# Performance work log

Measured on AMD Instinct MI355X. Metric: run time of the kernel, lower is better.

## Reference

```python
import jax, jax.numpy as jnp
import numpy as np

N, E, D, L = 50000, 800000, 128, 4


def setup_inputs() -> dict:
    key = jax.random.key(0)
    k0, k1, k2, k3 = jax.random.split(key, 4)
    x = jax.random.normal(k0, (N, D), dtype=jnp.float32)
    edge_index = jax.random.randint(k1, (2, E), 0, N, dtype=jnp.int32)
    # per-layer GCNConv weights [L, D, D] and biases [L, D]
    W = jax.random.normal(k2, (L, D, D), dtype=jnp.float32) * (1.0 / np.sqrt(D))
    b = jax.random.normal(k3, (L, D), dtype=jnp.float32) * 0.01
    batch_index = jnp.zeros((N,), dtype=jnp.int32)
    node_rankings = jnp.zeros((N,), dtype=jnp.int32)
    return {"x": x, "edge_index": edge_index, "batch_index": batch_index,
            "node_rankings": node_rankings, "W": W, "b": b}


def reference(x, edge_index, batch_index, node_rankings, W, b):
    # NullControl contributes 0; dropout_rate=0 / eval -> identity.
    n = x.shape[0]
    loops = jnp.arange(n, dtype=edge_index.dtype)
    row = jnp.concatenate([edge_index[0], loops])  # sources (with self-loops)
    col = jnp.concatenate([edge_index[1], loops])  # destinations
    # symmetric GCN normalization: deg over destinations, norm = d_i^-1/2 d_j^-1/2
    deg = jax.ops.segment_sum(jnp.ones_like(row, dtype=x.dtype), col, num_segments=n)
    dinv = jnp.where(deg > 0, jax.lax.rsqrt(deg), 0.0)
    norm = dinv[row] * dinv[col]  # [E+N]
    for l in range(W.shape[0]):
        h = x @ W[l]                      # [N, D] dense transform
        msg = h[row] * norm[:, None]      # [E+N, D] gathered, scaled messages
        agg = jax.ops.segment_sum(msg, col, num_segments=n)  # scatter-add
        x = jax.nn.relu(agg + b[l])       # control(=0) + bias + relu
    return x
```

## Files before the change

kernel.cpp:

```cpp
#include <hip/hip_runtime.h>

#define D 128
#define NLAYERS 4

typedef unsigned short ushort_t;
typedef unsigned int uint_t;
typedef __attribute__((ext_vector_type(8))) short short8;
typedef __attribute__((ext_vector_type(4))) float f32x4;

__device__ __forceinline__ ushort_t f2bf(float f) {
    uint_t u = __float_as_uint(f);
    u += 0x7FFFu + ((u >> 16) & 1u);
    return (ushort_t)(u >> 16);
}
__device__ __forceinline__ float bf_lo(uint_t u) {
    return __uint_as_float(u << 16);
}
__device__ __forceinline__ float bf_hi(uint_t u) {
    return __uint_as_float(u & 0xFFFF0000u);
}
__device__ __forceinline__ uint_t pack2(float a, float b) {
    return (uint_t)f2bf(a) | ((uint_t)f2bf(b) << 16);
}


__global__ void k_count_deg(const int* __restrict__ dsts, int E,
                            int* __restrict__ deg, int* __restrict__ slot) {
    int i = blockIdx.x * blockDim.x + threadIdx.x;
    if (i < E) slot[i] = atomicAdd(&deg[dsts[i]], 1);
}

__global__ void k_scan1(const int* __restrict__ deg, int n, int* __restrict__ out,
                        int* __restrict__ partials, float* __restrict__ dinv) {
    __shared__ int wsum[4];
    int tid = threadIdx.x;
    int base = blockIdx.x * 1024 + tid * 4;
    int d0 = (base + 0 < n) ? deg[base + 0] : 0;
    int d1 = (base + 1 < n) ? deg[base + 1] : 0;
    int d2 = (base + 2 < n) ? deg[base + 2] : 0;
    int d3 = (base + 3 < n) ? deg[base + 3] : 0;
    if (base + 0 < n) dinv[base + 0] = rsqrtf((float)(d0 + 1));
    if (base + 1 < n) dinv[base + 1] = rsqrtf((float)(d1 + 1));
    if (base + 2 < n) dinv[base + 2] = rsqrtf((float)(d2 + 1));
    if (base + 3 < n) dinv[base + 3] = rsqrtf((float)(d3 + 1));
    int s = d0 + d1 + d2 + d3;
    int lane = tid & 63;
    int incl = s;
    #pragma unroll
    for (int off = 1; off < 64; off <<= 1) {
        int y = __shfl_up(incl, off);
        if (lane >= off) incl += y;
    }
    int wid = tid >> 6;
    if (lane == 63) wsum[wid] = incl;
    __syncthreads();
    int wprev = 0;
    for (int w = 0; w < wid; w++) wprev += wsum[w];
    int excl = wprev + (incl - s);
    if (base + 0 < n) out[base + 0] = excl;
    if (base + 1 < n) out[base + 1] = excl + d0;
    if (base + 2 < n) out[base + 2] = excl + d0 + d1;
    if (base + 3 < n) out[base + 3] = excl + d0 + d1 + d2;
    if (tid == 255) partials[blockIdx.x] = wprev + incl;
}

__global__ void k_scan2(int* partials, int nb) {
    if (threadIdx.x == 0 && blockIdx.x == 0) {
        int acc = 0;
        for (int i = 0; i < nb; i++) { int t = partials[i]; partials[i] = acc; acc += t; }
    }
}

__global__ void k_scan3(int* __restrict__ row_ptr, const int* __restrict__ partials,
                        int n, int E) {
    int i = blockIdx.x * blockDim.x + threadIdx.x;
    if (i < n) row_ptr[i] += partials[i >> 10];
    if (i == 0) row_ptr[n] = E;
}

__global__ void k_place(const int* __restrict__ srcs, const int* __restrict__ dsts, int E,
                        const int* __restrict__ row_ptr, const int* __restrict__ slot,
                        const float* __restrict__ dinv, int2* __restrict__ ew) {
    int i = blockIdx.x * blockDim.x + threadIdx.x;
    if (i >= E) return;
    int c = dsts[i], r = srcs[i];
    int pos = row_ptr[c] + slot[i];
    int2 v;
    v.x = r;
    v.y = __float_as_int(dinv[r]);
    ew[pos] = v;
}

__global__ void k_wprep(const float* __restrict__ W, ushort_t* __restrict__ Wt_hi,
                        ushort_t* __restrict__ Wt_lo) {
    int t = blockIdx.x * 256 + threadIdx.x;
    int l = t >> 14;
    int k = (t >> 7) & 127;
    int nn = t & 127;
    float w = W[((size_t)l << 14) + k * 128 + nn];
    ushort_t hi = f2bf(w);
    float wf = __uint_as_float((uint_t)hi << 16);
    ushort_t lo = f2bf(w - wf);
    size_t o = ((size_t)l << 14) + nn * 128 + k;
    Wt_hi[o] = hi;
    Wt_lo[o] = lo;
}

__global__ void k_tobf16(const float* __restrict__ x, ushort_t* __restrict__ xh,
                         int total4) {
    int i = blockIdx.x * blockDim.x + threadIdx.x;
    if (i >= total4) return;
    float4 v = ((const float4*)x)[i];
    uint2 o;
    o.x = pack2(v.x, v.y);
    o.y = pack2(v.z, v.w);
    ((uint2*)xh)[i] = o;
}

__global__ __launch_bounds__(256) void k_aggregate(
    const ushort_t* __restrict__ xh, const int* __restrict__ row_ptr,
    const int2* __restrict__ ew, const float* __restrict__ dinv,
    ushort_t* __restrict__ s, int n) {
    int gwave = (blockIdx.x * 256 + threadIdx.x) >> 6;
    if (gwave >= n) return;
    int lane = threadIdx.x & 63;
    int sub = lane >> 4;
    int t = lane & 15;
    int node = gwave;
    float di = dinv[node];

    float acc[8];
    {
        uint4 v = *(const uint4*)(xh + (size_t)node * D + t * 8);
        float w = (sub == 0) ? di : 0.f;
        acc[0] = w * bf_lo(v.x); acc[1] = w * bf_hi(v.x);
        acc[2] = w * bf_lo(v.y); acc[3] = w * bf_hi(v.y);
        acc[4] = w * bf_lo(v.z); acc[5] = w * bf_hi(v.z);
        acc[6] = w * bf_lo(v.w); acc[7] = w * bf_hi(v.w);
    }
    int e = row_ptr[node], end = row_ptr[node + 1];
    for (; e + 16 <= end; e += 16) {
        int2 g0 = ew[e + sub];
        int2 g1 = ew[e + 4 + sub];
        int2 g2 = ew[e + 8 + sub];
        int2 g3 = ew[e + 12 + sub];
        uint4 v0 = *(const uint4*)(xh + (size_t)g0.x * D + t * 8);
        uint4 v1 = *(const uint4*)(xh + (size_t)g1.x * D + t * 8);
        uint4 v2 = *(const uint4*)(xh + (size_t)g2.x * D + t * 8);
        uint4 v3 = *(const uint4*)(xh + (size_t)g3.x * D + t * 8);
        float w0 = __int_as_float(g0.y);
        float w1 = __int_as_float(g1.y);
        float w2 = __int_as_float(g2.y);
        float w3 = __int_as_float(g3.y);
        acc[0] += w0 * bf_lo(v0.x); acc[1] += w0 * bf_hi(v0.x);
        acc[2] += w0 * bf_lo(v0.y); acc[3] += w0 * bf_hi(v0.y);
        acc[4] += w0 * bf_lo(v0.z); acc[5] += w0 * bf_hi(v0.z);
        acc[6] += w0 * bf_lo(v0.w); acc[7] += w0 * bf_hi(v0.w);
        acc[0] += w1 * bf_lo(v1.x); acc[1] += w1 * bf_hi(v1.x);
        acc[2] += w1 * bf_lo(v1.y); acc[3] += w1 * bf_hi(v1.y);
        acc[4] += w1 * bf_lo(v1.z); acc[5] += w1 * bf_hi(v1.z);
        acc[6] += w1 * bf_lo(v1.w); acc[7] += w1 * bf_hi(v1.w);
        acc[0] += w2 * bf_lo(v2.x); acc[1] += w2 * bf_hi(v2.x);
        acc[2] += w2 * bf_lo(v2.y); acc[3] += w2 * bf_hi(v2.y);
        acc[4] += w2 * bf_lo(v2.z); acc[5] += w2 * bf_hi(v2.z);
        acc[6] += w2 * bf_lo(v2.w); acc[7] += w2 * bf_hi(v2.w);
        acc[0] += w3 * bf_lo(v3.x); acc[1] += w3 * bf_hi(v3.x);
        acc[2] += w3 * bf_lo(v3.y); acc[3] += w3 * bf_hi(v3.y);
        acc[4] += w3 * bf_lo(v3.z); acc[5] += w3 * bf_hi(v3.z);
        acc[6] += w3 * bf_lo(v3.w); acc[7] += w3 * bf_hi(v3.w);
    }
    for (; e < end; e += 4) {
        int rem = end - e;
        int k = (sub < rem) ? sub : 0;
        int2 g = ew[e + k];
        float w = (sub < rem) ? __int_as_float(g.y) : 0.f;
        uint4 v = *(const uint4*)(xh + (size_t)g.x * D + t * 8);
        acc[0] += w * bf_lo(v.x); acc[1] += w * bf_hi(v.x);
        acc[2] += w * bf_lo(v.y); acc[3] += w * bf_hi(v.y);
        acc[4] += w * bf_lo(v.z); acc[5] += w * bf_hi(v.z);
        acc[6] += w * bf_lo(v.w); acc[7] += w * bf_hi(v.w);
    }
    #pragma unroll
    for (int q = 0; q < 8; q++) {
        acc[q] += __shfl_xor(acc[q], 16);
        acc[q] += __shfl_xor(acc[q], 32);
    }
    if (sub == 0) {
        ushort_t* dst = s + (size_t)node * D + t * 8;
        uint4 o;
        o.x = pack2(di * acc[0], di * acc[1]);
        o.y = pack2(di * acc[2], di * acc[3]);
        o.z = pack2(di * acc[4], di * acc[5]);
        o.w = pack2(di * acc[6], di * acc[7]);
        *(uint4*)dst = o;
    }
}

__global__ __launch_bounds__(256) void k_gemm_mfma(
    const ushort_t* __restrict__ A, const ushort_t* __restrict__ Wt_hi,
    const ushort_t* __restrict__ Wt_lo, const float* __restrict__ bias,
    float* __restrict__ out_f32, ushort_t* __restrict__ out_bf, int n) {
    int tid = threadIdx.x;
    int wave = tid >> 6;
    int lane = tid & 63;
    int lg = lane >> 4;
    int lr = lane & 15;
    int base_row = blockIdx.x * 128 + wave * 32;

    short8 a[2][4];
    #pragma unroll
    for (int st = 0; st < 2; st++) {
        int r = base_row + st * 16 + lr;
        if (r > n - 1) r = n - 1;
        const ushort_t* ap = A + (size_t)r * D + lg * 8;
        #pragma unroll
        for (int k0 = 0; k0 < 4; k0++)
            a[st][k0] = *(const short8*)(ap + k0 * 32);
    }

    f32x4 acc[2][8];
    #pragma unroll
    for (int st = 0; st < 2; st++)
        #pragma unroll
        for (int nt = 0; nt < 8; nt++)
            acc[st][nt] = (f32x4){0.f, 0.f, 0.f, 0.f};

    #pragma unroll
    for (int nt = 0; nt < 8; nt++) {
        const ushort_t* wh = Wt_hi + (size_t)(nt * 16 + lr) * D + lg * 8;
        const ushort_t* wl = Wt_lo + (size_t)(nt * 16 + lr) * D + lg * 8;
        #pragma unroll
        for (int k0 = 0; k0 < 4; k0++) {
            short8 bh = *(const short8*)(wh + k0 * 32);
            short8 bl = *(const short8*)(wl + k0 * 32);
            acc[0][nt] = __builtin_amdgcn_mfma_f32_16x16x32_bf16(a[0][k0], bh, acc[0][nt], 0, 0, 0);
            acc[0][nt] = __builtin_amdgcn_mfma_f32_16x16x32_bf16(a[0][k0], bl, acc[0][nt], 0, 0, 0);
            acc[1][nt] = __builtin_amdgcn_mfma_f32_16x16x32_bf16(a[1][k0], bh, acc[1][nt], 0, 0, 0);
            acc[1][nt] = __builtin_amdgcn_mfma_f32_16x16x32_bf16(a[1][k0], bl, acc[1][nt], 0, 0, 0);
        }
    }

    #pragma unroll
    for (int nt = 0; nt < 8; nt++) {
        int col = nt * 16 + lr;
        float bv = bias[col];
        #pragma unroll
        for (int st = 0; st < 2; st++) {
            #pragma unroll
            for (int r = 0; r < 4; r++) {
                int grow = base_row + st * 16 + lg * 4 + r;
                if (grow < n) {
                    float o = fmaxf(acc[st][nt][r] + bv, 0.f);
                    if (out_bf) out_bf[(size_t)grow * D + col] = f2bf(o);
                    else out_f32[(size_t)grow * D + col] = o;
                }
            }
        }
    }
}


extern "C" void kernel_launch(void* const* d_in, const int* in_sizes, int n_in,
                              void* d_out, int out_size, void* d_ws, size_t ws_size,
                              hipStream_t stream) {
    const float* x   = (const float*)d_in[0];
    const int* eidx  = (const int*)d_in[1];
    const float* W   = (const float*)d_in[4];
    const float* b   = (const float*)d_in[5];
    float* out       = (float*)d_out;

    const int N = in_sizes[0] / D;
    const int E = in_sizes[1] / 2;
    const int* srcs = eidx;
    const int* dsts = eidx + E;

    char* ws = (char*)d_ws;
    size_t off = 0;
    auto alloc = [&](size_t bytes) -> void* {
        void* p = ws + off;
        off = (off + bytes + 511) & ~(size_t)511;
        return p;
    };
    int*      deg      = (int*)alloc((size_t)N * 4);
    float*    dinv     = (float*)alloc((size_t)N * 4);
    int*      row_ptr  = (int*)alloc((size_t)(N + 1) * 4);
    int*      partials = (int*)alloc(256 * 4);
    int2*     ew       = (int2*)alloc((size_t)E * 8);
    ushort_t* s_buf    = (ushort_t*)alloc((size_t)N * D * 2);
    ushort_t* xh0      = (ushort_t*)alloc((size_t)N * D * 2);
    ushort_t* xh1      = (ushort_t*)alloc((size_t)N * D * 2);
    ushort_t* wt_hi    = (ushort_t*)alloc((size_t)NLAYERS * D * D * 2);
    ushort_t* wt_lo    = (ushort_t*)alloc((size_t)NLAYERS * D * D * 2);
    int*      slot     = (int*)s_buf;
    (void)ws_size; (void)n_in; (void)out_size;

    hipMemsetAsync(deg, 0, (size_t)N * 4, stream);

    int tE = (E + 255) / 256;
    int tN = (N + 255) / 256;
    int nbScan = (N + 1023) / 1024;

    k_count_deg<<<tE, 256, 0, stream>>>(dsts, E, deg, slot);
    k_scan1<<<nbScan, 256, 0, stream>>>(deg, N, row_ptr, partials, dinv);
    k_scan2<<<1, 64, 0, stream>>>(partials, nbScan);
    k_scan3<<<tN, 256, 0, stream>>>(row_ptr, partials, N, E);
    k_place<<<tE, 256, 0, stream>>>(srcs, dsts, E, row_ptr, slot, dinv, ew);
    k_wprep<<<(NLAYERS * D * D) / 256, 256, 0, stream>>>(W, wt_hi, wt_lo);

    int total4 = N * D / 4;
    k_tobf16<<<(total4 + 255) / 256, 256, 0, stream>>>(x, xh0, total4);

    int aggBlocks = (N + 3) / 4;
    int gemmBlocks = (N + 127) / 128;

    const ushort_t* xin = xh0;
    for (int l = 0; l < NLAYERS; l++) {
        k_aggregate<<<aggBlocks, 256, 0, stream>>>(xin, row_ptr, ew, dinv, s_buf, N);
        bool last = (l == NLAYERS - 1);
        ushort_t* xout = last ? nullptr : ((l & 1) ? xh0 : xh1);
        k_gemm_mfma<<<gemmBlocks, 256, 0, stream>>>(
            s_buf, wt_hi + (size_t)l * D * D, wt_lo + (size_t)l * D * D,
            b + (size_t)l * D, last ? out : nullptr, xout, N);
        xin = xout;
    }
}
```

Before: 387.2 us.

## Pre-scale features by dinv, pad CSR rows to multiples of four, fuse prep kernels

Features are stored pre-multiplied by the source node's dinv, and the GEMM epilogue applies dinv to its output. Edge weights therefore drop out and the CSR holds only 4-byte indices. Each row, including its self-loop, is padded to a multiple of four with a dummy zero row, so the aggregation can load four indices at once with an int4 and skip the per-edge multiply and tail masking. The scan, placement, weight prep and bf16 conversion kernels are merged into fewer launches. The cost is extra padded gathers of the zero row and slightly different bf16 rounding, since scaling now happens before quantisation.

```diff
diff --git a/kernel.cpp b/kernel.cpp
--- a/kernel.cpp
+++ b/kernel.cpp
@@ -30,20 +30,24 @@
     if (i < E) slot[i] = atomicAdd(&deg[dsts[i]], 1);
 }
 
-__global__ void k_scan1(const int* __restrict__ deg, int n, int* __restrict__ out,
+__global__ void k_scan1(const int* __restrict__ deg, int n, int* __restrict__ prow,
                         int* __restrict__ partials, float* __restrict__ dinv) {
     __shared__ int wsum[4];
     int tid = threadIdx.x;
     int base = blockIdx.x * 1024 + tid * 4;
-    int d0 = (base + 0 < n) ? deg[base + 0] : 0;
-    int d1 = (base + 1 < n) ? deg[base + 1] : 0;
-    int d2 = (base + 2 < n) ? deg[base + 2] : 0;
-    int d3 = (base + 3 < n) ? deg[base + 3] : 0;
-    if (base + 0 < n) dinv[base + 0] = rsqrtf((float)(d0 + 1));
-    if (base + 1 < n) dinv[base + 1] = rsqrtf((float)(d1 + 1));
-    if (base + 2 < n) dinv[base + 2] = rsqrtf((float)(d2 + 1));
-    if (base + 3 < n) dinv[base + 3] = rsqrtf((float)(d3 + 1));
-    int s = d0 + d1 + d2 + d3;
+    int g0 = (base + 0 < n) ? deg[base + 0] : -4;
+    int g1 = (base + 1 < n) ? deg[base + 1] : -4;
+    int g2 = (base + 2 < n) ? deg[base + 2] : -4;
+    int g3 = (base + 3 < n) ? deg[base + 3] : -4;
+    if (base + 0 < n) dinv[base + 0] = rsqrtf((float)(g0 + 1));
+    if (base + 1 < n) dinv[base + 1] = rsqrtf((float)(g1 + 1));
+    if (base + 2 < n) dinv[base + 2] = rsqrtf((float)(g2 + 1));
+    if (base + 3 < n) dinv[base + 3] = rsqrtf((float)(g3 + 1));
+    int p0 = (g0 + 4) & ~3;
+    int p1 = (g1 + 4) & ~3;
+    int p2 = (g2 + 4) & ~3;
+    int p3 = (g3 + 4) & ~3;
+    int s = p0 + p1 + p2 + p3;
     int lane = tid & 63;
     int incl = s;
     #pragma unroll
@@ -57,69 +61,84 @@
     int wprev = 0;
     for (int w = 0; w < wid; w++) wprev += wsum[w];
     int excl = wprev + (incl - s);
-    if (base + 0 < n) out[base + 0] = excl;
-    if (base + 1 < n) out[base + 1] = excl + d0;
-    if (base + 2 < n) out[base + 2] = excl + d0 + d1;
-    if (base + 3 < n) out[base + 3] = excl + d0 + d1 + d2;
+    if (base + 0 < n) prow[base + 0] = excl;
+    if (base + 1 < n) prow[base + 1] = excl + p0;
+    if (base + 2 < n) prow[base + 2] = excl + p0 + p1;
+    if (base + 3 < n) prow[base + 3] = excl + p0 + p1 + p2;
     if (tid == 255) partials[blockIdx.x] = wprev + incl;
 }
 
-__global__ void k_scan2(int* partials, int nb) {
-    if (threadIdx.x == 0 && blockIdx.x == 0) {
-        int acc = 0;
-        for (int i = 0; i < nb; i++) { int t = partials[i]; partials[i] = acc; acc += t; }
-    }
-}
-
-__global__ void k_scan3(int* __restrict__ row_ptr, const int* __restrict__ partials,
-                        int n, int E) {
+__global__ void k_scan23(int* __restrict__ prow, const int* __restrict__ partials,
+                         int n, int nb) {
     int i = blockIdx.x * blockDim.x + threadIdx.x;
-    if (i < n) row_ptr[i] += partials[i >> 10];
-    if (i == 0) row_ptr[n] = E;
-}
-
-__global__ void k_place(const int* __restrict__ srcs, const int* __restrict__ dsts, int E,
-                        const int* __restrict__ row_ptr, const int* __restrict__ slot,
-                        const float* __restrict__ dinv, int2* __restrict__ ew) {
-    int i = blockIdx.x * blockDim.x + threadIdx.x;
-    if (i >= E) return;
-    int c = dsts[i], r = srcs[i];
-    int pos = row_ptr[c] + slot[i];
-    int2 v;
-    v.x = r;
-    v.y = __float_as_int(dinv[r]);
-    ew[pos] = v;
-}
-
-__global__ void k_wprep(const float* __restrict__ W, ushort_t* __restrict__ Wt_hi,
-                        ushort_t* __restrict__ Wt_lo) {
-    int t = blockIdx.x * 256 + threadIdx.x;
-    int l = t >> 14;
-    int k = (t >> 7) & 127;
-    int nn = t & 127;
-    float w = W[((size_t)l << 14) + k * 128 + nn];
-    ushort_t hi = f2bf(w);
-    float wf = __uint_as_float((uint_t)hi << 16);
-    ushort_t lo = f2bf(w - wf);
-    size_t o = ((size_t)l << 14) + nn * 128 + k;
-    Wt_hi[o] = hi;
-    Wt_lo[o] = lo;
-}
-
-__global__ void k_tobf16(const float* __restrict__ x, ushort_t* __restrict__ xh,
-                         int total4) {
-    int i = blockIdx.x * blockDim.x + threadIdx.x;
-    if (i >= total4) return;
-    float4 v = ((const float4*)x)[i];
-    uint2 o;
-    o.x = pack2(v.x, v.y);
-    o.y = pack2(v.z, v.w);
-    ((uint2*)xh)[i] = o;
+    int chunk = (blockIdx.x * blockDim.x) >> 10;
+    int pre = 0;
+    for (int j = 0; j < chunk; j++) pre += partials[j];
+    if (i < n) prow[i] += pre;
+    if (i == 0) {
+        int tot = 0;
+        for (int j = 0; j < nb; j++) tot += partials[j];
+        prow[n] = tot;
+    }
+}
+
+__global__ void k_prep(const int* __restrict__ srcs, const int* __restrict__ dsts,
+                       const int* __restrict__ deg, const int* __restrict__ slot,
+                       const int* __restrict__ prow, const float* __restrict__ dinv,
+                       const float* __restrict__ x, const float* __restrict__ W,
+                       int* __restrict__ ewi, ushort_t* __restrict__ xs0,
+                       ushort_t* __restrict__ xs1, ushort_t* __restrict__ Wt_hi,
+                       ushort_t* __restrict__ Wt_lo, int n, int E,
+                       int B1, int B2, int B3, int B4) {
+    int b = blockIdx.x;
+    int tid = threadIdx.x;
+    if (b < B1) {
+        int i = b * 256 + tid;
+        if (i < E) {
+            int c = dsts[i];
+            ewi[prow[c] + 1 + slot[i]] = srcs[i];
+        }
+    } else if (b < B2) {
+        int i = (b - B1) * 256 + tid;
+        if (i < n) {
+            int base = prow[i];
+            int len = deg[i] + 1;
+            int plen = (deg[i] + 4) & ~3;
+            ewi[base] = i;
+            for (int j = len; j < plen; j++) ewi[base + j] = n;
+        }
+    } else if (b < B3) {
+        int idx = (b - B2) * 256 + tid;
+        if (idx < n * (D / 4)) {
+            int row = idx >> 5;
+            float di = dinv[row];
+            float4 v = ((const float4*)x)[idx];
+            uint2 o;
+            o.x = pack2(di * v.x, di * v.y);
+            o.y = pack2(di * v.z, di * v.w);
+            ((uint2*)xs0)[idx] = o;
+        }
+    } else if (b < B4) {
+        int t = (b - B3) * 256 + tid;
+        int l = t >> 14;
+        int k = (t >> 7) & 127;
+        int nn = t & 127;
+        float w = W[((size_t)l << 14) + k * 128 + nn];
+        ushort_t hi = f2bf(w);
+        float wf = __uint_as_float((uint_t)hi << 16);
+        ushort_t lo = f2bf(w - wf);
+        size_t o = ((size_t)l << 14) + nn * 128 + k;
+        Wt_hi[o] = hi;
+        Wt_lo[o] = lo;
+    } else {
+        if (tid < 128) xs0[(size_t)n * D + tid] = 0;
+        else xs1[(size_t)n * D + (tid - 128)] = 0;
+    }
 }
 
 __global__ __launch_bounds__(256) void k_aggregate(
-    const ushort_t* __restrict__ xh, const int* __restrict__ row_ptr,
-    const int2* __restrict__ ew, const float* __restrict__ dinv,
+    const ushort_t* __restrict__ xs, const int* __restrict__ prow,
+    const int* __restrict__ ewi, const float* __restrict__ dinv,
     ushort_t* __restrict__ s, int n) {
     int gwave = (blockIdx.x * 256 + threadIdx.x) >> 6;
     if (gwave >= n) return;
@@ -129,56 +148,38 @@
     int node = gwave;
     float di = dinv[node];
 
-    float acc[8];
-    {
-        uint4 v = *(const uint4*)(xh + (size_t)node * D + t * 8);
-        float w = (sub == 0) ? di : 0.f;
-        acc[0] = w * bf_lo(v.x); acc[1] = w * bf_hi(v.x);
-        acc[2] = w * bf_lo(v.y); acc[3] = w * bf_hi(v.y);
-        acc[4] = w * bf_lo(v.z); acc[5] = w * bf_hi(v.z);
-        acc[6] = w * bf_lo(v.w); acc[7] = w * bf_hi(v.w);
-    }
-    int e = row_ptr[node], end = row_ptr[node + 1];
+    float acc[8] = {0.f, 0.f, 0.f, 0.f, 0.f, 0.f, 0.f, 0.f};
+    int e = prow[node], end = prow[node + 1];
     for (; e + 16 <= end; e += 16) {
-        int2 g0 = ew[e + sub];
-        int2 g1 = ew[e + 4 + sub];
-        int2 g2 = ew[e + 8 + sub];
-        int2 g3 = ew[e + 12 + sub];
-        uint4 v0 = *(const uint4*)(xh + (size_t)g0.x * D + t * 8);
-        uint4 v1 = *(const uint4*)(xh + (size_t)g1.x * D + t * 8);
-        uint4 v2 = *(const uint4*)(xh + (size_t)g2.x * D + t * 8);
-        uint4 v3 = *(const uint4*)(xh + (size_t)g3.x * D + t * 8);
-        float w0 = __int_as_float(g0.y);
-        float w1 = __int_as_float(g1.y);
-        float w2 = __int_as_float(g2.y);
-        float w3 = __int_as_float(g3.y);
-        acc[0] += w0 * bf_lo(v0.x); acc[1] += w0 * bf_hi(v0.x);
-        acc[2] += w0 * bf_lo(v0.y); acc[3] += w0 * bf_hi(v0.y);
-        acc[4] += w0 * bf_lo(v0.z); acc[5] += w0 * bf_hi(v0.z);
-        acc[6] += w0 * bf_lo(v0.w); acc[7] += w0 * bf_hi(v0.w);
-        acc[0] += w1 * bf_lo(v1.x); acc[1] += w1 * bf_hi(v1.x);
-        acc[2] += w1 * bf_lo(v1.y); acc[3] += w1 * bf_hi(v1.y);
-        acc[4] += w1 * bf_lo(v1.z); acc[5] += w1 * bf_hi(v1.z);
-        acc[6] += w1 * bf_lo(v1.w); acc[7] += w1 * bf_hi(v1.w);
-        acc[0] += w2 * bf_lo(v2.x); acc[1] += w2 * bf_hi(v2.x);
-        acc[2] += w2 * bf_lo(v2.y); acc[3] += w2 * bf_hi(v2.y);
-        acc[4] += w2 * bf_lo(v2.z); acc[5] += w2 * bf_hi(v2.z);
-        acc[6] += w2 * bf_lo(v2.w); acc[7] += w2 * bf_hi(v2.w);
-        acc[0] += w3 * bf_lo(v3.x); acc[1] += w3 * bf_hi(v3.x);
-        acc[2] += w3 * bf_lo(v3.y); acc[3] += w3 * bf_hi(v3.y);
-        acc[4] += w3 * bf_lo(v3.z); acc[5] += w3 * bf_hi(v3.z);
-        acc[6] += w3 * bf_lo(v3.w); acc[7] += w3 * bf_hi(v3.w);
+        int4 gg = *(const int4*)(ewi + e + sub * 4);
+        uint4 v0 = *(const uint4*)(xs + (size_t)gg.x * D + t * 8);
+        uint4 v1 = *(const uint4*)(xs + (size_t)gg.y * D + t * 8);
+        uint4 v2 = *(const uint4*)(xs + (size_t)gg.z * D + t * 8);
+        uint4 v3 = *(const uint4*)(xs + (size_t)gg.w * D + t * 8);
+        acc[0] += bf_lo(v0.x); acc[1] += bf_hi(v0.x);
+        acc[2] += bf_lo(v0.y); acc[3] += bf_hi(v0.y);
+        acc[4] += bf_lo(v0.z); acc[5] += bf_hi(v0.z);
+        acc[6] += bf_lo(v0.w); acc[7] += bf_hi(v0.w);
+        acc[0] += bf_lo(v1.x); acc[1] += bf_hi(v1.x);
+        acc[2] += bf_lo(v1.y); acc[3] += bf_hi(v1.y);
+        acc[4] += bf_lo(v1.z); acc[5] += bf_hi(v1.z);
+        acc[6] += bf_lo(v1.w); acc[7] += bf_hi(v1.w);
+        acc[0] += bf_lo(v2.x); acc[1] += bf_hi(v2.x);
+        acc[2] += bf_lo(v2.y); acc[3] += bf_hi(v2.y);
+        acc[4] += bf_lo(v2.z); acc[5] += bf_hi(v2.z);
+        acc[6] += bf_lo(v2.w); acc[7] += bf_hi(v2.w);
+        acc[0] += bf_lo(v3.x); acc[1] += bf_hi(v3.x);
+        acc[2] += bf_lo(v3.y); acc[3] += bf_hi(v3.y);
+        acc[4] += bf_lo(v3.z); acc[5] += bf_hi(v3.z);
+        acc[6] += bf_lo(v3.w); acc[7] += bf_hi(v3.w);
     }
     for (; e < end; e += 4) {
-        int rem = end - e;
-        int k = (sub < rem) ? sub : 0;
-        int2 g = ew[e + k];
-        float w = (sub < rem) ? __int_as_float(g.y) : 0.f;
-        uint4 v = *(const uint4*)(xh + (size_t)g.x * D + t * 8);
-        acc[0] += w * bf_lo(v.x); acc[1] += w * bf_hi(v.x);
-        acc[2] += w * bf_lo(v.y); acc[3] += w * bf_hi(v.y);
-        acc[4] += w * bf_lo(v.z); acc[5] += w * bf_hi(v.z);
-        acc[6] += w * bf_lo(v.w); acc[7] += w * bf_hi(v.w);
+        int g = ewi[e + sub];
+        uint4 v = *(const uint4*)(xs + (size_t)g * D + t * 8);
+        acc[0] += bf_lo(v.x); acc[1] += bf_hi(v.x);
+        acc[2] += bf_lo(v.y); acc[3] += bf_hi(v.y);
+        acc[4] += bf_lo(v.z); acc[5] += bf_hi(v.z);
+        acc[6] += bf_lo(v.w); acc[7] += bf_hi(v.w);
     }
     #pragma unroll
     for (int q = 0; q < 8; q++) {
@@ -199,7 +200,8 @@
 __global__ __launch_bounds__(256) void k_gemm_mfma(
     const ushort_t* __restrict__ A, const ushort_t* __restrict__ Wt_hi,
     const ushort_t* __restrict__ Wt_lo, const float* __restrict__ bias,
-    float* __restrict__ out_f32, ushort_t* __restrict__ out_bf, int n) {
+    const float* __restrict__ dinv, float* __restrict__ out_f32,
+    ushort_t* __restrict__ out_bf, int n) {
     int tid = threadIdx.x;
     int wave = tid >> 6;
     int lane = tid & 63;
@@ -251,7 +253,7 @@
                 int grow = base_row + st * 16 + lg * 4 + r;
                 if (grow < n) {
                     float o = fmaxf(acc[st][nt][r] + bv, 0.f);
-                    if (out_bf) out_bf[(size_t)grow * D + col] = f2bf(o);
+                    if (out_bf) out_bf[(size_t)grow * D + col] = f2bf(dinv[grow] * o);
                     else out_f32[(size_t)grow * D + col] = o;
                 }
             }
@@ -283,12 +285,12 @@
     };
     int*      deg      = (int*)alloc((size_t)N * 4);
     float*    dinv     = (float*)alloc((size_t)N * 4);
-    int*      row_ptr  = (int*)alloc((size_t)(N + 1) * 4);
+    int*      prow     = (int*)alloc((size_t)(N + 1) * 4);
     int*      partials = (int*)alloc(256 * 4);
-    int2*     ew       = (int2*)alloc((size_t)E * 8);
+    int*      ewi      = (int*)alloc((size_t)(E + 4 * N) * 4);
     ushort_t* s_buf    = (ushort_t*)alloc((size_t)N * D * 2);
-    ushort_t* xh0      = (ushort_t*)alloc((size_t)N * D * 2);
-    ushort_t* xh1      = (ushort_t*)alloc((size_t)N * D * 2);
+    ushort_t* xh0      = (ushort_t*)alloc(((size_t)N + 1) * D * 2);
+    ushort_t* xh1      = (ushort_t*)alloc(((size_t)N + 1) * D * 2);
     ushort_t* wt_hi    = (ushort_t*)alloc((size_t)NLAYERS * D * D * 2);
     ushort_t* wt_lo    = (ushort_t*)alloc((size_t)NLAYERS * D * D * 2);
     int*      slot     = (int*)s_buf;
@@ -301,26 +303,28 @@
     int nbScan = (N + 1023) / 1024;
 
     k_count_deg<<<tE, 256, 0, stream>>>(dsts, E, deg, slot);
-    k_scan1<<<nbScan, 256, 0, stream>>>(deg, N, row_ptr, partials, dinv);
-    k_scan2<<<1, 64, 0, stream>>>(partials, nbScan);
-    k_scan3<<<tN, 256, 0, stream>>>(row_ptr, partials, N, E);
-    k_place<<<tE, 256, 0, stream>>>(srcs, dsts, E, row_ptr, slot, dinv, ew);
-    k_wprep<<<(NLAYERS * D * D) / 256, 256, 0, stream>>>(W, wt_hi, wt_lo);
-
-    int total4 = N * D / 4;
-    k_tobf16<<<(total4 + 255) / 256, 256, 0, stream>>>(x, xh0, total4);
+    k_scan1<<<nbScan, 256, 0, stream>>>(deg, N, prow, partials, dinv);
+    k_scan23<<<tN, 256, 0, stream>>>(prow, partials, N, nbScan);
+
+    int B1 = tE;
+    int B2 = B1 + tN;
+    int B3 = B2 + (N * (D / 4) + 255) / 256;
+    int B4 = B3 + (NLAYERS * D * D) / 256;
+    k_prep<<<B4 + 1, 256, 0, stream>>>(srcs, dsts, deg, slot, prow, dinv, x, W,
+                                       ewi, xh0, xh1, wt_hi, wt_lo, N, E,
+                                       B1, B2, B3, B4);
 
     int aggBlocks = (N + 3) / 4;
     int gemmBlocks = (N + 127) / 128;
 
     const ushort_t* xin = xh0;
     for (int l = 0; l < NLAYERS; l++) {
-        k_aggregate<<<aggBlocks, 256, 0, stream>>>(xin, row_ptr, ew, dinv, s_buf, N);
+        k_aggregate<<<aggBlocks, 256, 0, stream>>>(xin, prow, ewi, dinv, s_buf, N);
         bool last = (l == NLAYERS - 1);
         ushort_t* xout = last ? nullptr : ((l & 1) ? xh0 : xh1);
         k_gemm_mfma<<<gemmBlocks, 256, 0, stream>>>(
             s_buf, wt_hi + (size_t)l * D * D, wt_lo + (size_t)l * D * D,
-            b + (size_t)l * D, last ? out : nullptr, xout, N);
+            b + (size_t)l * D, dinv, last ? out : nullptr, xout, N);
         xin = xout;
     }
 }
```

New measurement: 390.8 us. Within noise of the previous version (+0.9%).
